# Optimization experiments

Hardware: AMD Instinct MI355X
Metric: run time of the kernel (lower is better)

Reference implementation:

```python
import jax, jax.numpy as jnp
import numpy as np

EPS = 1e-5
NUM_GROUPS = 32
NUM_HEADS = 8

def group_norm(x, w, b):
    # x: (B, C, H, W), 32 groups, affine per-channel
    B, C, H, W = x.shape
    xg = x.reshape(B, NUM_GROUPS, C // NUM_GROUPS, H, W)
    mu = xg.mean(axis=(2, 3, 4), keepdims=True)
    var = xg.var(axis=(2, 3, 4), keepdims=True)
    xn = ((xg - mu) * jax.lax.rsqrt(var + EPS)).reshape(B, C, H, W)
    return xn * w[None, :, None, None] + b[None, :, None, None]

def conv1x1(x, w, b):
    # 1x1 conv == per-pixel linear; w: (out, in), x: (B, C, H, W)
    return jnp.einsum('oc,bchw->bohw', w, x) + b[None, :, None, None]

def setup_inputs() -> dict:
    key = jax.random.key(0)
    ks = jax.random.split(key, 4)
    B, C, H, W = 2, 512, 64, 64
    s = 1.0 / np.sqrt(C)
    return {
        'x': jax.random.normal(ks[0], (B, C, H, W), jnp.float32),
        'gn_w': jnp.ones((C,), jnp.float32),
        'gn_b': jnp.zeros((C,), jnp.float32),
        'wq': jax.random.normal(ks[1], (C, C), jnp.float32) * s,
        'bq': jnp.zeros((C,), jnp.float32),
        'wkv': jax.random.normal(ks[2], (2 * C, C), jnp.float32) * s,
        'bkv': jnp.zeros((2 * C,), jnp.float32),
        'wo': jax.random.normal(ks[3], (C, C), jnp.float32) * s,
        'bo': jnp.zeros((C,), jnp.float32),
    }

def reference(x, gn_w, gn_b, wq, bq, wkv, bkv, wo, bo):
    B, C, H, W = x.shape
    hd = C // NUM_HEADS  # head_dim
    residual = x
    x_norm = group_norm(x, gn_w, gn_b)
    q = conv1x1(x_norm, wq, bq).reshape(B, NUM_HEADS, hd, H * W)
    kv = conv1x1(x_norm, wkv, bkv)
    k, v = jnp.split(kv, 2, axis=1)
    k = k.reshape(B, NUM_HEADS, hd, H * W)
    v = v.reshape(B, NUM_HEADS, hd, H * W)
    scale = hd ** (-0.5)
    attn = jnp.einsum('bhdi,bhdj->bhij', q, k) * scale
    attn = jax.nn.softmax(attn, axis=-1)
    out = jnp.einsum('bhij,bhdj->bhdi', attn, v).reshape(B, C, H, W)
    out = conv1x1(out, wo, bo)
    return out + residual
```

## Files before the change

kernel.cpp:

```cpp
#include <hip/hip_runtime.h>
#include <cmath>

typedef __bf16 bf16x8 __attribute__((ext_vector_type(8)));
typedef __bf16 bf16x4 __attribute__((ext_vector_type(4)));
typedef float  f32x4  __attribute__((ext_vector_type(4)));
typedef unsigned uint2_ev __attribute__((ext_vector_type(2)));

static __device__ __forceinline__ f32x4 mfma16(bf16x8 a, bf16x8 b, f32x4 c) {
    return __builtin_amdgcn_mfma_f32_16x16x32_bf16(a, b, c, 0, 0, 0);
}

static __device__ __forceinline__ float fast_exp2(float x) {
#if __has_builtin(__builtin_amdgcn_exp2f)
    return __builtin_amdgcn_exp2f(x);
#else
    return exp2f(x);
#endif
}

static __device__ __forceinline__ void quad_swap(unsigned &a, unsigned &b) {
#if __has_builtin(__builtin_amdgcn_permlane32_swap) && __has_builtin(__builtin_amdgcn_permlane16_swap)
    uint2_ev r32 = __builtin_amdgcn_permlane32_swap(a, b, false, false);
    uint2_ev r16 = __builtin_amdgcn_permlane16_swap(r32[0], r32[1], false, false);
    a = r16[0]; b = r16[1];
#else
    asm volatile("v_permlane32_swap_b32 %0, %1\n\t"
                 "v_permlane16_swap_b32 %0, %1"
                 : "+v"(a), "+v"(b));
#endif
}

static __device__ __forceinline__ void gload_lds16(const void* g, void* l) {
    __builtin_amdgcn_global_load_lds((const __attribute__((address_space(1))) void*)g,
                                     (__attribute__((address_space(3))) void*)l, 16, 0, 0);
}

#define OFF_STATS 0
#define OFF_BEFF  1024
#define OFF_W     16384
#define OFF_XNT   (4u*1024*1024)
#define OFF_QKT   (OFF_XNT + 8u*1024*1024)
#define OFF_V     (OFF_QKT + 16u*1024*1024)
#define OFF_OP    (OFF_V + 8u*1024*1024)
#define CHUNK_O   4194304u
#define CHUNK_L   65536u

__global__ __launch_bounds__(256) void gn_fuse(const float* __restrict__ x,
                                               float* __restrict__ stats,
                                               __bf16* __restrict__ xT) {
    int p0 = blockIdx.x * 64, c0 = blockIdx.y * 64, b = blockIdx.z;
    int tid = threadIdx.x, lane = tid & 63, wave = tid >> 6;
    __shared__ float t[64][69];
    __shared__ float red[4][8];
    float acc_s[4] = {0.f,0.f,0.f,0.f}, acc_ss[4] = {0.f,0.f,0.f,0.f};
    #pragma unroll
    for (int i = 0; i < 16; ++i) {
        int cc = i*4 + wave;
        float val = x[((size_t)(b*512 + c0 + cc) << 12) + p0 + lane];
        t[cc][lane] = val;
        acc_s[i>>2]  += val;
        acc_ss[i>>2] += val*val;
    }
    #pragma unroll
    for (int g = 0; g < 4; ++g) {
        #pragma unroll
        for (int off = 1; off < 64; off <<= 1) {
            acc_s[g]  += __shfl_xor(acc_s[g],  off);
            acc_ss[g] += __shfl_xor(acc_ss[g], off);
        }
    }
    if (lane == 0) {
        #pragma unroll
        for (int g = 0; g < 4; ++g) { red[wave][g*2] = acc_s[g]; red[wave][g*2+1] = acc_ss[g]; }
    }
    __syncthreads();
    if (tid < 8) {
        float v0 = red[0][tid] + red[1][tid] + red[2][tid] + red[3][tid];
        int g = (b << 5) + (c0 >> 4) + (tid >> 1);
        atomicAdd(&stats[g*2 + (tid & 1)], v0);
    }
    #pragma unroll
    for (int i = 0; i < 16; ++i) {
        int pp = i*4 + wave;
        xT[((size_t)(b*4096 + p0 + pp) << 9) + c0 + lane] = (__bf16)t[lane][pp];
    }
}

__global__ __launch_bounds__(256) void prep_w(const float* __restrict__ wq,
                                              const float* __restrict__ wkv,
                                              const float* __restrict__ wo,
                                              const float* __restrict__ bq,
                                              const float* __restrict__ bkv,
                                              const float* __restrict__ stats,
                                              const float* __restrict__ gw,
                                              const float* __restrict__ gb,
                                              __bf16* __restrict__ wS,
                                              __bf16* __restrict__ wo_bf,
                                              float* __restrict__ beff) {
    const int b = blockIdx.y, bx = blockIdx.x;
    const int tid = threadIdx.x, lane = tid & 63, wave = tid >> 6;
    if (bx >= 48) {
        if (b) return;
        int r0 = (bx - 48) * 32;
        #pragma unroll
        for (int ps = 0; ps < 8; ++ps) {
            int row = r0 + ps*4 + wave;
            __bf16 obuf[8];
            #pragma unroll
            for (int e = 0; e < 8; ++e) obuf[e] = (__bf16)wo[(size_t)row*512 + lane*8 + e];
            *(bf16x8*)&wo_bf[(size_t)row*512 + lane*8] = *(bf16x8*)obuf;
        }
        return;
    }
    __shared__ float sS[512], sT[512];
    for (int c = tid; c < 512; c += 256) {
        int g = (b << 5) + (c >> 4);
        float mu   = stats[g*2] * (1.f/65536.f);
        float var  = stats[g*2+1] * (1.f/65536.f) - mu*mu;
        float rstd = rsqrtf(var + 1e-5f);
        float s = rstd * gw[c];
        sS[c] = s;
        sT[c] = gb[c] - mu * s;
    }
    __syncthreads();
    int r0 = bx * 32;
    #pragma unroll
    for (int ps = 0; ps < 8; ++ps) {
        int row = r0 + ps*4 + wave;
        const float* Wrow = (row < 512) ? (wq + (size_t)row*512) : (wkv + (size_t)(row-512)*512);
        float bias0 = (row < 512) ? bq[row] : bkv[row - 512];
        float bp = 0.f;
        __bf16 obuf[8];
        #pragma unroll
        for (int e = 0; e < 8; ++e) {
            int c = lane*8 + e;
            float wv_ = Wrow[c];
            obuf[e] = (__bf16)(wv_ * sS[c]);
            bp += wv_ * sT[c];
        }
        *(bf16x8*)&wS[((size_t)b*1536 + row)*512 + lane*8] = *(bf16x8*)obuf;
        #pragma unroll
        for (int off = 1; off < 64; off <<= 1) bp += __shfl_xor(bp, off);
        if (lane == 0) beff[b*1536 + row] = bias0 + bp;
    }
}

__global__ __launch_bounds__(256) void gemm128_kernel(
    const __bf16* __restrict__ A, const __bf16* __restrict__ B,
    const float* __restrict__ bias, int nsplit,
    float scale0, void* __restrict__ out,
    int N, int K, long long strideA, long long strideB, long long strideO, int biasStride) {
    const int bz = blockIdx.z;
    A += strideA * bz;
    B += strideB * bz;
    const float* bb = bias + (size_t)bz * biasStride;
    const int m0 = blockIdx.x * 128, n0 = blockIdx.y * 128;
    const int tid = threadIdx.x, lane = tid & 63, wave = tid >> 6;
    const int quad = lane >> 4, l16 = lane & 15;
    const int wm = (wave >> 1) * 64, wn = (wave & 1) * 64;

    __shared__ __attribute__((aligned(16))) __bf16 lds_a[128][40];
    __shared__ __attribute__((aligned(16))) __bf16 lds_b[128][40];

    f32x4 acc[4][4];
    #pragma unroll
    for (int mt = 0; mt < 4; ++mt)
        #pragma unroll
        for (int nt = 0; nt < 4; ++nt)
            #pragma unroll
            for (int r = 0; r < 4; ++r) acc[mt][nt][r] = 0.f;

    const int row_s = tid >> 2;
    const int kc    = (tid & 3) << 3;

    uint4 ra0, ra1, rb0, rb1;
    const __bf16* Abase = A + (size_t)(m0 + row_s) * K + kc;
    const __bf16* Bbase = B + (size_t)(n0 + row_s) * K + kc;
    ra0 = *(const uint4*)Abase;
    ra1 = *(const uint4*)(Abase + (size_t)64 * K);
    rb0 = *(const uint4*)Bbase;
    rb1 = *(const uint4*)(Bbase + (size_t)64 * K);

    for (int kt = 0; kt < K; kt += 32) {
        *(uint4*)&lds_a[row_s][kc]      = ra0;
        *(uint4*)&lds_a[row_s + 64][kc] = ra1;
        *(uint4*)&lds_b[row_s][kc]      = rb0;
        *(uint4*)&lds_b[row_s + 64][kc] = rb1;
        __syncthreads();
        if (kt + 32 < K) {
            ra0 = *(const uint4*)(Abase + kt + 32);
            ra1 = *(const uint4*)(Abase + kt + 32 + (size_t)64 * K);
            rb0 = *(const uint4*)(Bbase + kt + 32);
            rb1 = *(const uint4*)(Bbase + kt + 32 + (size_t)64 * K);
        }
        bf16x8 af[4], bfr[4];
        #pragma unroll
        for (int mt = 0; mt < 4; ++mt)
            af[mt] = *(const bf16x8*)&lds_a[wm + mt*16 + l16][quad*8];
        #pragma unroll
        for (int nt = 0; nt < 4; ++nt)
            bfr[nt] = *(const bf16x8*)&lds_b[wn + nt*16 + l16][quad*8];
        #pragma unroll
        for (int mt = 0; mt < 4; ++mt)
            #pragma unroll
            for (int nt = 0; nt < 4; ++nt)
                acc[mt][nt] = mfma16(af[mt], bfr[nt], acc[mt][nt]);
        __syncthreads();
    }

    #pragma unroll
    for (int mt = 0; mt < 4; ++mt) {
        const int mrow = m0 + wm + mt*16 + quad*4;
        #pragma unroll
        for (int nt = 0; nt < 4; ++nt) {
            const int ncol = n0 + wn + nt*16 + l16;
            #pragma unroll
            for (int r = 0; r < 4; ++r) {
                const int m = mrow + r;
                float val = acc[mt][nt][r] + bb[ncol];
                if (ncol < nsplit) val *= scale0;
                ((__bf16*)out)[(size_t)strideO * bz + (size_t)m * N + ncol] = (__bf16)val;
            }
        }
    }
}

template<int OUT_F32, int HAS_RES>
__global__ __launch_bounds__(256) void gemm64_kernel(
    const __bf16* __restrict__ A, const __bf16* __restrict__ B,
    const float* __restrict__ bias, const float* __restrict__ res,
    void* __restrict__ out,
    int N, int K, long long strideA, long long strideB, long long strideO, int biasStride) {
    const int bz = blockIdx.z;
    A += strideA * bz;
    B += strideB * bz;
    const float* bb = bias + (size_t)bz * biasStride;
    const int m0 = blockIdx.x * 64, n0 = blockIdx.y * 128;
    const int tid = threadIdx.x, lane = tid & 63, wave = tid >> 6;
    const int quad = lane >> 4, l16 = lane & 15;
    const int wn = wave * 32;

    __shared__ __attribute__((aligned(16))) __bf16 lds_a[64][40];
    __shared__ __attribute__((aligned(16))) __bf16 lds_b[128][40];

    f32x4 acc[4][2];
    #pragma unroll
    for (int mt = 0; mt < 4; ++mt)
        #pragma unroll
        for (int nt = 0; nt < 2; ++nt)
            #pragma unroll
            for (int r = 0; r < 4; ++r) acc[mt][nt][r] = 0.f;

    const int row_s = tid >> 2;
    const int kc    = (tid & 3) << 3;

    uint4 ra0, rb0, rb1;
    const __bf16* Abase = A + (size_t)(m0 + row_s) * K + kc;
    const __bf16* Bbase = B + (size_t)(n0 + row_s) * K + kc;
    ra0 = *(const uint4*)Abase;
    rb0 = *(const uint4*)Bbase;
    rb1 = *(const uint4*)(Bbase + (size_t)64 * K);

    for (int kt = 0; kt < K; kt += 32) {
        *(uint4*)&lds_a[row_s][kc]      = ra0;
        *(uint4*)&lds_b[row_s][kc]      = rb0;
        *(uint4*)&lds_b[row_s + 64][kc] = rb1;
        __syncthreads();
        if (kt + 32 < K) {
            ra0 = *(const uint4*)(Abase + kt + 32);
            rb0 = *(const uint4*)(Bbase + kt + 32);
            rb1 = *(const uint4*)(Bbase + kt + 32 + (size_t)64 * K);
        }
        bf16x8 af[4], bfr[2];
        #pragma unroll
        for (int mt = 0; mt < 4; ++mt)
            af[mt] = *(const bf16x8*)&lds_a[mt*16 + l16][quad*8];
        #pragma unroll
        for (int nt = 0; nt < 2; ++nt)
            bfr[nt] = *(const bf16x8*)&lds_b[wn + nt*16 + l16][quad*8];
        #pragma unroll
        for (int mt = 0; mt < 4; ++mt)
            #pragma unroll
            for (int nt = 0; nt < 2; ++nt)
                acc[mt][nt] = mfma16(af[mt], bfr[nt], acc[mt][nt]);
        __syncthreads();
    }

    #pragma unroll
    for (int mt = 0; mt < 4; ++mt) {
        const int mrow = m0 + mt*16 + quad*4;
        #pragma unroll
        for (int nt = 0; nt < 2; ++nt) {
            const int ncol = n0 + wn + nt*16 + l16;
            #pragma unroll
            for (int r = 0; r < 4; ++r) {
                const int m = mrow + r;
                float val = acc[mt][nt][r] + bb[m];
                const size_t idx = (size_t)strideO * bz + (size_t)m * N + ncol;
                if constexpr (HAS_RES) val += res[idx];
                if constexpr (OUT_F32) ((float*)out)[idx] = val;
                else ((__bf16*)out)[idx] = (__bf16)val;
            }
        }
    }
}

template<int NCH>
__global__ __launch_bounds__(256, 3) void attn_kernel(const __bf16* __restrict__ qkT,
                                                      const __bf16* __restrict__ v,
                                                      __bf16* __restrict__ attnT,
                                                      __bf16* __restrict__ Opart,
                                                      float* __restrict__ Lpart) {
    const int b = blockIdx.y >> 3, h = blockIdx.y & 7;
    const int chunk = (NCH > 1) ? blockIdx.z : 0;
    int NITER, kt0;
    if constexpr (NCH == 3) {
        NITER = (chunk == 0) ? 22 : 21;
        kt0   = (chunk == 0) ? 0 : (chunk == 1 ? 1408 : 2752);
    } else {
        NITER = 64 / NCH;
        kt0   = chunk * (4096 / NCH);
    }
    const int tid = threadIdx.x;
    const int wave = tid >> 6, lane = tid & 63;
    const int quad = lane >> 4, l16 = lane & 15;
    const int qbase = blockIdx.x * 256 + wave * 64;

    const __bf16* qkTb = qkT + ((size_t)b << 22);
    const __bf16* vb   = v   + ((size_t)b << 21);

    __shared__ __attribute__((aligned(16))) __bf16 lds_k[2][64][64];
    __shared__ __attribute__((aligned(16))) __bf16 lds_v[2][64][64];

    bf16x8 aq[4][2];
    #pragma unroll
    for (int mt = 0; mt < 4; ++mt) {
        const __bf16* qrow = qkTb + (size_t)(qbase + mt*16 + l16) * 1024 + h*64 + quad*8;
        aq[mt][0] = *(const bf16x8*)qrow;
        aq[mt][1] = *(const bf16x8*)(qrow + 32);
    }
    f32x4 o[4][5];
    #pragma unroll
    for (int mt = 0; mt < 4; ++mt)
        #pragma unroll
        for (int dt = 0; dt < 5; ++dt)
            #pragma unroll
            for (int r = 0; r < 4; ++r) o[mt][dt][r] = 0.f;
    const f32x4 kZero = {0.f, 0.f, 0.f, 0.f};

    bf16x8 onesb;
    #pragma unroll
    for (int e = 0; e < 8; ++e) onesb[e] = (__bf16)1.0f;

    const int myrow = (wave << 3) + (lane >> 3);
    const int mych  = ((lane & 7) ^ (myrow & 7)) << 3;
    const __bf16* kgb = qkTb + (size_t)myrow * 1024 + 512 + h*64 + mych;
    const __bf16* vgb = vb + ((size_t)(h*64 + myrow) << 12) + mych;

    auto stage = [&](int buf, int kt) {
        char* kb = (char*)(&lds_k[buf][0][0]) + (wave << 10);
        char* vp = (char*)(&lds_v[buf][0][0]) + (wave << 10);
        const __bf16* kg = kgb + (size_t)kt * 1024;
        const __bf16* vg = vgb + kt;
        gload_lds16(kg,                       kb);
        gload_lds16(kg + 32*1024,             kb + 4096);
        gload_lds16(vg,                       vp);
        gload_lds16(vg + ((size_t)32 << 12),  vp + 4096);
    };

    stage(0, kt0);

    for (int it = 0; it < NITER; ++it) {
        __syncthreads();
        const int cur = it & 1;
        if (it + 1 < NITER) stage(cur ^ 1, kt0 + (it + 1) * 64);

        #pragma unroll
        for (int kh = 0; kh < 2; ++kh) {
            unsigned pd[4][4];
            #pragma unroll
            for (int j = 0; j < 2; ++j) {
                const int nt = kh*2 + j;
                const int kr = nt*16 + l16;
                bf16x8 bk0 = *(const bf16x8*)&lds_k[cur][kr][( quad      ^ (l16 & 7)) * 8];
                bf16x8 bk1 = *(const bf16x8*)&lds_k[cur][kr][((4 + quad) ^ (l16 & 7)) * 8];
                #pragma unroll
                for (int mt = 0; mt < 4; ++mt) {
                    f32x4 s = mfma16(bk1, aq[mt][1], mfma16(bk0, aq[mt][0], kZero));
                    f32x4 p;
                    #pragma unroll
                    for (int r = 0; r < 4; ++r) p[r] = fast_exp2(s[r]);
                    bf16x4 pb = __builtin_convertvector(p, bf16x4);
                    union { bf16x4 v; unsigned d[2]; } u; u.v = pb;
                    pd[mt][j*2]     = u.d[0];
                    pd[mt][j*2 + 1] = u.d[1];
                }
            }
            bf16x8 pa[4];
            #pragma unroll
            for (int mt = 0; mt < 4; ++mt) {
                unsigned x0 = pd[mt][0], x1 = pd[mt][1];
                unsigned y0 = pd[mt][2], y1 = pd[mt][3];
                quad_swap(x0, y0);
                quad_swap(x1, y1);
                union { unsigned d[4]; bf16x8 v; } u;
                u.d[0] = x0; u.d[1] = x1; u.d[2] = y0; u.d[3] = y1;
                pa[mt] = u.v;
            }
            #pragma unroll
            for (int dt = 0; dt < 4; ++dt) {
                bf16x8 bv = *(const bf16x8*)&lds_v[cur][dt*16 + l16][((kh*4 + quad) ^ (l16 & 7)) * 8];
                #pragma unroll
                for (int mt = 0; mt < 4; ++mt)
                    o[mt][dt] = mfma16(pa[mt], bv, o[mt][dt]);
            }
            #pragma unroll
            for (int mt = 0; mt < 4; ++mt)
                o[mt][4] = mfma16(pa[mt], onesb, o[mt][4]);
        }
    }

    if constexpr (NCH > 1) {
        __bf16* Ob = Opart + (size_t)chunk * CHUNK_O;
        #pragma unroll
        for (int mt = 0; mt < 4; ++mt)
            #pragma unroll
            for (int dt = 0; dt < 4; ++dt)
                #pragma unroll
                for (int r = 0; r < 4; ++r) {
                    size_t row = (size_t)b * 4096 + qbase + mt*16 + quad*4 + r;
                    Ob[(row << 9) + (h << 6) + dt*16 + l16] = (__bf16)o[mt][dt][r];
                }
        if (l16 == 0) {
            #pragma unroll
            for (int mt = 0; mt < 4; ++mt)
                #pragma unroll
                for (int r = 0; r < 4; ++r) {
                    int p = qbase + mt*16 + quad*4 + r;
                    Lpart[(size_t)chunk * CHUNK_L + (size_t)(((b*8 + h)) << 12) + p] = o[mt][4][r];
                }
        }
    } else {
        #pragma unroll
        for (int mt = 0; mt < 4; ++mt) {
            float inv[4];
            #pragma unroll
            for (int r = 0; r < 4; ++r)
                inv[r] = 1.f / __shfl(o[mt][4][r], lane & 48);
            #pragma unroll
            for (int dt = 0; dt < 4; ++dt)
                #pragma unroll
                for (int r = 0; r < 4; ++r) {
                    size_t row = (size_t)b * 4096 + qbase + mt*16 + quad*4 + r;
                    attnT[(row << 9) + (h << 6) + dt*16 + l16] = (__bf16)(o[mt][dt][r] * inv[r]);
                }
        }
    }
}

template<int NCH>
__global__ __launch_bounds__(256) void attn_combine(const __bf16* __restrict__ Opart,
                                                    const float* __restrict__ Lpart,
                                                    __bf16* __restrict__ attnT) {
    int i = blockIdx.x * 256 + threadIdx.x;
    int c4 = i & 127;
    int p  = (i >> 7) & 4095;
    int b  = i >> 19;
    int h  = c4 >> 4;
    size_t lidx = (size_t)((b*8 + h) << 12) + p;
    float l = 0.f;
    #pragma unroll
    for (int ch = 0; ch < NCH; ++ch) l += Lpart[(size_t)ch * CHUNK_L + lidx];
    float inv = 1.f / l;
    size_t oi = ((size_t)(b*4096 + p) << 9) + c4*4;
    float acc[4] = {0.f, 0.f, 0.f, 0.f};
    #pragma unroll
    for (int ch = 0; ch < NCH; ++ch) {
        bf16x4 ov = *(const bf16x4*)&Opart[(size_t)ch * CHUNK_O + oi];
        #pragma unroll
        for (int r = 0; r < 4; ++r) acc[r] += (float)ov[r];
    }
    bf16x4 rv;
    #pragma unroll
    for (int r = 0; r < 4; ++r) rv[r] = (__bf16)(acc[r] * inv);
    *(bf16x4*)&attnT[oi] = rv;
}

extern "C" void kernel_launch(void* const* d_in, const int* in_sizes, int n_in,
                              void* d_out, int out_size, void* d_ws, size_t ws_size,
                              hipStream_t stream) {
    const float* x   = (const float*)d_in[0];
    const float* gnw = (const float*)d_in[1];
    const float* gnb = (const float*)d_in[2];
    const float* wq  = (const float*)d_in[3];
    const float* bq  = (const float*)d_in[4];
    const float* wkv = (const float*)d_in[5];
    const float* bkv = (const float*)d_in[6];
    const float* wo  = (const float*)d_in[7];
    const float* bo  = (const float*)d_in[8];
    float* out = (float*)d_out;

    char* ws = (char*)d_ws;
    float*  stats  = (float*)(ws + OFF_STATS);
    float*  beff   = (float*)(ws + OFF_BEFF);
    __bf16* wS     = (__bf16*)(ws + OFF_W);
    __bf16* wo_bf  = wS + 2u*1536*512;
    __bf16* xT     = (__bf16*)(ws + OFF_XNT);
    __bf16* qkT    = (__bf16*)(ws + OFF_QKT);
    __bf16* vv     = (__bf16*)(ws + OFF_V);
    __bf16* Opart  = (__bf16*)(ws + OFF_OP);
    __bf16* attnT  = xT;

    const size_t need3 = (size_t)OFF_OP + 3u * (CHUNK_O * 2 + CHUNK_L * 4);
    const size_t need2 = (size_t)OFF_OP + 2u * (CHUNK_O * 2 + CHUNK_L * 4);
    const int nch = (ws_size >= need3) ? 3 : (ws_size >= need2 ? 2 : 1);
    float* Lpart = (float*)(ws + OFF_OP + (size_t)nch * CHUNK_O * 2);

    hipMemsetAsync(stats, 0, 512, stream);
    gn_fuse<<<dim3(64, 8, 2), 256, 0, stream>>>(x, stats, xT);
    prep_w<<<dim3(64, 2), 256, 0, stream>>>(wq, wkv, wo, bq, bkv, stats, gnw, gnb,
                                            wS, wo_bf, beff);

    const long long S  = 2097152LL;
    const long long S2 = 4194304LL;
    const long long SW = 1536LL*512;
    gemm128_kernel<<<dim3(32, 8, 2), 256, 0, stream>>>(
        xT, wS, beff, 512, 0.125f * 1.44269504f, qkT, 1024, 512, S, SW, S2, 1536);
    gemm64_kernel<0,0><<<dim3(8, 32, 2), 256, 0, stream>>>(
        wS + 1024*512, xT, beff + 1024, nullptr, vv, 4096, 512, SW, S, S, 1536);

    if (nch == 3) {
        attn_kernel<3><<<dim3(16, 16, 3), 256, 0, stream>>>(qkT, vv, nullptr, Opart, Lpart);
        attn_combine<3><<<4096, 256, 0, stream>>>(Opart, Lpart, attnT);
    } else if (nch == 2) {
        attn_kernel<2><<<dim3(16, 16, 2), 256, 0, stream>>>(qkT, vv, nullptr, Opart, Lpart);
        attn_combine<2><<<4096, 256, 0, stream>>>(Opart, Lpart, attnT);
    } else {
        attn_kernel<1><<<dim3(16, 16, 1), 256, 0, stream>>>(qkT, vv, attnT, nullptr, nullptr);
    }

    gemm64_kernel<1,1><<<dim3(8, 32, 2), 256, 0, stream>>>(
        wo_bf, attnT, bo, x, out, 4096, 512, 0, S, S, 0);
}
```

Baseline: 218.5 us.

## Vectorize GN transpose and combine, compute softmax row sums with VALU

The group-norm transpose kernel now reads x as float4 and writes the transposed activations as 8-wide bf16 stores. The attention kernel stops running an extra MFMA against a ones vector for the softmax denominator. It accumulates the exp values in registers instead and reduces them with cross-lane shuffles, which frees MFMA issue slots and accumulator registers but adds VALU adds to the inner loop. The combine kernel now handles 8 bf16 per thread with half as many blocks. The row sums are taken from fp32 values before the bf16 rounding, so they differ slightly from the earlier sums of the rounded probabilities.

New measurement: 277.1 us. 26.8% more time.

```diff
diff --git a/kernel.cpp b/kernel.cpp
--- a/kernel.cpp
+++ b/kernel.cpp
@@ -50,16 +50,18 @@
                                                __bf16* __restrict__ xT) {
     int p0 = blockIdx.x * 64, c0 = blockIdx.y * 64, b = blockIdx.z;
     int tid = threadIdx.x, lane = tid & 63, wave = tid >> 6;
-    __shared__ float t[64][69];
+    __shared__ float t[64][68];
     __shared__ float red[4][8];
     float acc_s[4] = {0.f,0.f,0.f,0.f}, acc_ss[4] = {0.f,0.f,0.f,0.f};
-    #pragma unroll
-    for (int i = 0; i < 16; ++i) {
-        int cc = i*4 + wave;
-        float val = x[((size_t)(b*512 + c0 + cc) << 12) + p0 + lane];
-        t[cc][lane] = val;
-        acc_s[i>>2]  += val;
-        acc_ss[i>>2] += val*val;
+    const int rr = tid >> 4;
+    const int p4 = (tid & 15) * 4;
+    #pragma unroll
+    for (int i = 0; i < 4; ++i) {
+        int cc = rr + 16*i;
+        float4 v = *(const float4*)&x[((size_t)(b*512 + c0 + cc) << 12) + p0 + p4];
+        *(float4*)&t[cc][p4] = v;
+        acc_s[i]  += v.x + v.y + v.z + v.w;
+        acc_ss[i] += v.x*v.x + v.y*v.y + v.z*v.z + v.w*v.w;
     }
     #pragma unroll
     for (int g = 0; g < 4; ++g) {
@@ -79,10 +81,14 @@
         int g = (b << 5) + (c0 >> 4) + (tid >> 1);
         atomicAdd(&stats[g*2 + (tid & 1)], v0);
     }
-    #pragma unroll
-    for (int i = 0; i < 16; ++i) {
-        int pp = i*4 + wave;
-        xT[((size_t)(b*4096 + p0 + pp) << 9) + c0 + lane] = (__bf16)t[lane][pp];
+    const int ch = tid & 7;
+    #pragma unroll
+    for (int w = 0; w < 2; ++w) {
+        int pp = (tid >> 3) + 32*w;
+        __bf16 ob[8];
+        #pragma unroll
+        for (int e = 0; e < 8; ++e) ob[e] = (__bf16)t[ch*8 + e][pp];
+        *(bf16x8*)&xT[((size_t)(b*4096 + p0 + pp) << 9) + c0 + ch*8] = *(bf16x8*)ob;
     }
 }
 
@@ -339,18 +345,15 @@
         aq[mt][0] = *(const bf16x8*)qrow;
         aq[mt][1] = *(const bf16x8*)(qrow + 32);
     }
-    f32x4 o[4][5];
+    f32x4 o[4][4];
     #pragma unroll
     for (int mt = 0; mt < 4; ++mt)
         #pragma unroll
-        for (int dt = 0; dt < 5; ++dt)
+        for (int dt = 0; dt < 4; ++dt)
             #pragma unroll
             for (int r = 0; r < 4; ++r) o[mt][dt][r] = 0.f;
+    float lsum[4] = {0.f, 0.f, 0.f, 0.f};
     const f32x4 kZero = {0.f, 0.f, 0.f, 0.f};
-
-    bf16x8 onesb;
-    #pragma unroll
-    for (int e = 0; e < 8; ++e) onesb[e] = (__bf16)1.0f;
 
     const int myrow = (wave << 3) + (lane >> 3);
     const int mych  = ((lane & 7) ^ (myrow & 7)) << 3;
@@ -387,10 +390,11 @@
                 #pragma unroll
                 for (int mt = 0; mt < 4; ++mt) {
                     f32x4 s = mfma16(bk1, aq[mt][1], mfma16(bk0, aq[mt][0], kZero));
-                    f32x4 p;
+                    f32x4 pv;
                     #pragma unroll
-                    for (int r = 0; r < 4; ++r) p[r] = fast_exp2(s[r]);
-                    bf16x4 pb = __builtin_convertvector(p, bf16x4);
+                    for (int r = 0; r < 4; ++r) pv[r] = fast_exp2(s[r]);
+                    lsum[mt] += (pv[0] + pv[1]) + (pv[2] + pv[3]);
+                    bf16x4 pb = __builtin_convertvector(pv, bf16x4);
                     union { bf16x4 v; unsigned d[2]; } u; u.v = pb;
                     pd[mt][j*2]     = u.d[0];
                     pd[mt][j*2 + 1] = u.d[1];
@@ -414,10 +418,16 @@
                 for (int mt = 0; mt < 4; ++mt)
                     o[mt][dt] = mfma16(pa[mt], bv, o[mt][dt]);
             }
-            #pragma unroll
-            for (int mt = 0; mt < 4; ++mt)
-                o[mt][4] = mfma16(pa[mt], onesb, o[mt][4]);
-        }
+        }
+    }
+
+    float fsum[4];
+    #pragma unroll
+    for (int mt = 0; mt < 4; ++mt) {
+        float fs = lsum[mt];
+        fs += __shfl_xor(fs, 16);
+        fs += __shfl_xor(fs, 32);
+        fsum[mt] = fs;
     }
 
     if constexpr (NCH > 1) {
@@ -431,14 +441,12 @@
                     size_t row = (size_t)b * 4096 + qbase + mt*16 + quad*4 + r;
                     Ob[(row << 9) + (h << 6) + dt*16 + l16] = (__bf16)o[mt][dt][r];
                 }
-        if (l16 == 0) {
-            #pragma unroll
-            for (int mt = 0; mt < 4; ++mt)
-                #pragma unroll
-                for (int r = 0; r < 4; ++r) {
-                    int p = qbase + mt*16 + quad*4 + r;
-                    Lpart[(size_t)chunk * CHUNK_L + (size_t)(((b*8 + h)) << 12) + p] = o[mt][4][r];
-                }
+        if (lane < 16) {
+            #pragma unroll
+            for (int mt = 0; mt < 4; ++mt) {
+                int pq = qbase + mt*16 + lane;
+                Lpart[(size_t)chunk * CHUNK_L + (size_t)(((b*8 + h)) << 12) + pq] = fsum[mt];
+            }
         }
     } else {
         #pragma unroll
@@ -446,7 +454,7 @@
             float inv[4];
             #pragma unroll
             for (int r = 0; r < 4; ++r)
-                inv[r] = 1.f / __shfl(o[mt][4][r], lane & 48);
+                inv[r] = 1.f / __shfl(fsum[mt], (quad << 2) + r);
             #pragma unroll
             for (int dt = 0; dt < 4; ++dt)
                 #pragma unroll
@@ -463,27 +471,27 @@
                                                     const float* __restrict__ Lpart,
                                                     __bf16* __restrict__ attnT) {
     int i = blockIdx.x * 256 + threadIdx.x;
-    int c4 = i & 127;
-    int p  = (i >> 7) & 4095;
-    int b  = i >> 19;
-    int h  = c4 >> 4;
+    int c8 = i & 63;
+    int p  = (i >> 6) & 4095;
+    int b  = i >> 18;
+    int h  = c8 >> 3;
     size_t lidx = (size_t)((b*8 + h) << 12) + p;
     float l = 0.f;
     #pragma unroll
     for (int ch = 0; ch < NCH; ++ch) l += Lpart[(size_t)ch * CHUNK_L + lidx];
     float inv = 1.f / l;
-    size_t oi = ((size_t)(b*4096 + p) << 9) + c4*4;
-    float acc[4] = {0.f, 0.f, 0.f, 0.f};
+    size_t oi = ((size_t)(b*4096 + p) << 9) + c8*8;
+    float acc[8] = {0.f,0.f,0.f,0.f,0.f,0.f,0.f,0.f};
     #pragma unroll
     for (int ch = 0; ch < NCH; ++ch) {
-        bf16x4 ov = *(const bf16x4*)&Opart[(size_t)ch * CHUNK_O + oi];
-        #pragma unroll
-        for (int r = 0; r < 4; ++r) acc[r] += (float)ov[r];
-    }
-    bf16x4 rv;
-    #pragma unroll
-    for (int r = 0; r < 4; ++r) rv[r] = (__bf16)(acc[r] * inv);
-    *(bf16x4*)&attnT[oi] = rv;
+        bf16x8 ov = *(const bf16x8*)&Opart[(size_t)ch * CHUNK_O + oi];
+        #pragma unroll
+        for (int r = 0; r < 8; ++r) acc[r] += (float)ov[r];
+    }
+    bf16x8 rv;
+    #pragma unroll
+    for (int r = 0; r < 8; ++r) rv[r] = (__bf16)(acc[r] * inv);
+    *(bf16x8*)&attnT[oi] = rv;
 }
 
 extern "C" void kernel_launch(void* const* d_in, const int* in_sizes, int n_in,
@@ -531,10 +539,10 @@
 
     if (nch == 3) {
         attn_kernel<3><<<dim3(16, 16, 3), 256, 0, stream>>>(qkT, vv, nullptr, Opart, Lpart);
-        attn_combine<3><<<4096, 256, 0, stream>>>(Opart, Lpart, attnT);
+        attn_combine<3><<<2048, 256, 0, stream>>>(Opart, Lpart, attnT);
     } else if (nch == 2) {
         attn_kernel<2><<<dim3(16, 16, 2), 256, 0, stream>>>(qkT, vv, nullptr, Opart, Lpart);
-        attn_combine<2><<<4096, 256, 0, stream>>>(Opart, Lpart, attnT);
+        attn_combine<2><<<2048, 256, 0, stream>>>(Opart, Lpart, attnT);
     } else {
         attn_kernel<1><<<dim3(16, 16, 1), 256, 0, stream>>>(qkT, vv, attnT, nullptr, nullptr);
     }
```
